# Performance work log

Measured on AMD Instinct MI355X. Metric: run time of the kernel, lower is better.

The kernel has to match this reference:

```python
import jax, jax.numpy as jnp
import numpy as np

NBITS = 4
QMAX = 2 ** (NBITS - 1) - 1   # 7
QMIN = -(2 ** (NBITS - 1))    # -8


def quantize_weight(W):
    # Brevitas-style symmetric per-tensor int4 weight quantization with STE.
    scale = jnp.max(jnp.abs(W)) / QMAX
    q = jnp.clip(jnp.round(W / scale), QMIN, QMAX) * scale
    # straight-through estimator (no-op for fwd-only, kept for parity)
    return W + jax.lax.stop_gradient(q - W)


def setup_inputs() -> dict:
    key = jax.random.key(0)
    k1, k2, k3 = jax.random.split(key, 3)
    x = jax.random.normal(k1, (8192, 4, 16, 16, 16), dtype=jnp.float32)
    W = jax.random.normal(k2, (4, 2048), dtype=jnp.float32) * 0.02
    b = jax.random.normal(k3, (4,), dtype=jnp.float32) * 0.01
    return {"x": x, "W": W, "b": b}


def reference(x, W, b):
    B, C, D, H, Wd = x.shape
    # MaxPool3d(kernel=2, stride=2): reshape-and-reduce (dims are divisible by 2)
    pooled = x.reshape(B, C, D // 2, 2, H // 2, 2, Wd // 2, 2).max(axis=(3, 5, 7))
    flat = pooled.reshape(B, -1)                      # [B, 2048]
    Wq = quantize_weight(W)                           # int4-dequantized weight
    logits = jnp.einsum("bf,of->bo", flat, Wq) + b    # [B, 4]
    return jax.nn.softmax(logits, axis=1)
```

## Files before the change

kernel.cpp:

```cpp
#include <hip/hip_runtime.h>
#include <math.h>

__global__ __launch_bounds__(1024) void quant_w_kernel(
        const float* __restrict__ W, float* __restrict__ wqt ) {
    __shared__ float smax[16];
    __shared__ float sscale;
    const int t = threadIdx.x;
    const float4 v0 = ((const float4*)W)[t];
    const float4 v1 = ((const float4*)W)[t + 1024];

    float m = fmaxf(
        fmaxf(fmaxf(fabsf(v0.x), fabsf(v0.y)), fmaxf(fabsf(v0.z), fabsf(v0.w))),
        fmaxf(fmaxf(fabsf(v1.x), fabsf(v1.y)), fmaxf(fabsf(v1.z), fabsf(v1.w))));
    #pragma unroll
    for (int off = 32; off; off >>= 1) m = fmaxf(m, __shfl_xor(m, off));
    if ((t & 63) == 0) smax[t >> 6] = m;
    __syncthreads();
    if (t == 0) {
        float M = smax[0];
        #pragma unroll
        for (int i = 1; i < 16; ++i) M = fmaxf(M, smax[i]);
        sscale = M / 7.0f;
    }
    __syncthreads();
    const float scale = sscale;

#define QSTORE(val, idx)                                              \
    {                                                                 \
        const int i_ = (idx);                                         \
        const int o_ = i_ >> 11;             \
        const int f_ = i_ & 2047;                        \
        float q_ = rintf((val) / scale);    \
        q_ = fminf(fmaxf(q_, -8.0f), 7.0f);                           \
        wqt[f_ * 4 + o_] = q_ * scale;                                \
    }
    const int i0 = t << 2;
    QSTORE(v0.x, i0 + 0); QSTORE(v0.y, i0 + 1);
    QSTORE(v0.z, i0 + 2); QSTORE(v0.w, i0 + 3);
    QSTORE(v1.x, i0 + 4096); QSTORE(v1.y, i0 + 4097);
    QSTORE(v1.z, i0 + 4098); QSTORE(v1.w, i0 + 4099);
#undef QSTORE
}

__global__ __launch_bounds__(256) void fused_pool_linear_softmax(
        const float* __restrict__ x,
        const float* __restrict__ wqt,
        const float* __restrict__ bias,
        float* __restrict__ out) {
    const int t  = threadIdx.x;
    const int wv = t >> 6;
    const int l  = t & 63;
    const int b  = (blockIdx.x << 2) + wv;

    const float* __restrict__ p = x + (size_t)b * 16384 + (l << 2);
    const int hodd = (l >> 2) & 1;
    const int f0   = hodd * 64 + (l >> 3) * 8 + ((l & 3) << 1);
    const float* __restrict__ wp = wqt + f0 * 4;

    float4 acc = make_float4(0.f, 0.f, 0.f, 0.f);

    #pragma unroll 4
    for (int it = 0; it < 16; ++it) {
        const float4 v0 = *(const float4*)(p);
        const float4 v1 = *(const float4*)(p + 256);
        const float4 v2 = *(const float4*)(p + 512);
        const float4 v3 = *(const float4*)(p + 768);
        p += 1024;

        const float aA = fmaxf(fmaxf(v0.x, v0.y), fmaxf(v1.x, v1.y));
        const float bA = fmaxf(fmaxf(v0.z, v0.w), fmaxf(v1.z, v1.w));
        const float aB = fmaxf(fmaxf(v2.x, v2.y), fmaxf(v3.x, v3.y));
        const float bB = fmaxf(fmaxf(v2.z, v2.w), fmaxf(v3.z, v3.w));

        const float saA = __shfl_xor(aA, 4);
        const float sbA = __shfl_xor(bA, 4);
        const float saB = __shfl_xor(aB, 4);
        const float sbB = __shfl_xor(bB, 4);

        const float p0 = hodd ? fmaxf(aB, saB) : fmaxf(aA, saA);
        const float p1 = hodd ? fmaxf(bB, sbB) : fmaxf(bA, sbA);

        const float4 w0 = *(const float4*)(wp);
        const float4 w1 = *(const float4*)(wp + 4);
        wp += 512;

        acc.x = fmaf(p0, w0.x, fmaf(p1, w1.x, acc.x));
        acc.y = fmaf(p0, w0.y, fmaf(p1, w1.y, acc.y));
        acc.z = fmaf(p0, w0.z, fmaf(p1, w1.z, acc.z));
        acc.w = fmaf(p0, w0.w, fmaf(p1, w1.w, acc.w));
    }

    #pragma unroll
    for (int off = 32; off; off >>= 1) {
        acc.x += __shfl_xor(acc.x, off);
        acc.y += __shfl_xor(acc.y, off);
        acc.z += __shfl_xor(acc.z, off);
        acc.w += __shfl_xor(acc.w, off);
    }

    if (l == 0) {
        const float4 bi = *(const float4*)bias;
        const float l0 = acc.x + bi.x, l1 = acc.y + bi.y,
                    l2 = acc.z + bi.z, l3 = acc.w + bi.w;
        const float m  = fmaxf(fmaxf(l0, l1), fmaxf(l2, l3));
        const float e0 = expf(l0 - m), e1 = expf(l1 - m),
                    e2 = expf(l2 - m), e3 = expf(l3 - m);
        const float inv = 1.0f / (e0 + e1 + e2 + e3);
        *(float4*)(out + (size_t)b * 4) =
            make_float4(e0 * inv, e1 * inv, e2 * inv, e3 * inv);
    }
}

extern "C" void kernel_launch(void* const* d_in, const int* in_sizes, int n_in,
                              void* d_out, int out_size, void* d_ws, size_t ws_size,
                              hipStream_t stream) {
    const float* x    = (const float*)d_in[0];
    const float* W    = (const float*)d_in[1];
    const float* bias = (const float*)d_in[2];
    float* out = (float*)d_out;
    float* wqt = (float*)d_ws;

    quant_w_kernel<<<1, 1024, 0, stream>>>(W, wqt);
    fused_pool_linear_softmax<<<2048, 256, 0, stream>>>(x, wqt, bias, out);
}
```

Before: 682.6 us.

## Fuse weight quantization into main kernel with per-block LDS weight copy

```diff
diff --git a/kernel.cpp b/kernel.cpp
--- a/kernel.cpp
+++ b/kernel.cpp
@@ -1,61 +1,57 @@
 #include <hip/hip_runtime.h>
 #include <math.h>
 
-__global__ __launch_bounds__(1024) void quant_w_kernel(
-        const float* __restrict__ W, float* __restrict__ wqt ) {
-    __shared__ float smax[16];
-    __shared__ float sscale;
+__global__ __launch_bounds__(512) void fused_all(
+        const float* __restrict__ x,
+        const float* __restrict__ W,
+        const float* __restrict__ bias,
+        float* __restrict__ out) {
+    __shared__ float wlds[2048 * 4];
+    __shared__ float smax[8];
+
     const int t = threadIdx.x;
-    const float4 v0 = ((const float4*)W)[t];
-    const float4 v1 = ((const float4*)W)[t + 1024];
+    const int l = t & 63;
 
-    float m = fmaxf(
-        fmaxf(fmaxf(fabsf(v0.x), fabsf(v0.y)), fmaxf(fabsf(v0.z), fabsf(v0.w))),
-        fmaxf(fmaxf(fabsf(v1.x), fabsf(v1.y)), fmaxf(fabsf(v1.z), fabsf(v1.w))));
+    float4 wv[4];
+    float m = 0.0f;
+    #pragma unroll
+    for (int i = 0; i < 4; ++i) {
+        wv[i] = ((const float4*)W)[t + 512 * i];
+        m = fmaxf(m, fmaxf(fmaxf(fabsf(wv[i].x), fabsf(wv[i].y)),
+                           fmaxf(fabsf(wv[i].z), fabsf(wv[i].w))));
+    }
     #pragma unroll
     for (int off = 32; off; off >>= 1) m = fmaxf(m, __shfl_xor(m, off));
-    if ((t & 63) == 0) smax[t >> 6] = m;
+    if (l == 0) smax[t >> 6] = m;
     __syncthreads();
-    if (t == 0) {
-        float M = smax[0];
-        #pragma unroll
-        for (int i = 1; i < 16; ++i) M = fmaxf(M, smax[i]);
-        sscale = M / 7.0f;
-    }
-    __syncthreads();
-    const float scale = sscale;
+    float M = smax[0];
+    #pragma unroll
+    for (int i = 1; i < 8; ++i) M = fmaxf(M, smax[i]);
+    const float scale = M / 7.0f;
 
-#define QSTORE(val, idx)                                              \
+#define QSTORE(val, gidx)                                             \
     {                                                                 \
-        const int i_ = (idx);                                         \
-        const int o_ = i_ >> 11;             \
-        const int f_ = i_ & 2047;                        \
+        const int g_ = (gidx);                                        \
         float q_ = rintf((val) / scale);    \
         q_ = fminf(fmaxf(q_, -8.0f), 7.0f);                           \
-        wqt[f_ * 4 + o_] = q_ * scale;                                \
+        wlds[(g_ & 2047) * 4 + (g_ >> 11)] = q_ * scale;              \
     }
-    const int i0 = t << 2;
-    QSTORE(v0.x, i0 + 0); QSTORE(v0.y, i0 + 1);
-    QSTORE(v0.z, i0 + 2); QSTORE(v0.w, i0 + 3);
-    QSTORE(v1.x, i0 + 4096); QSTORE(v1.y, i0 + 4097);
-    QSTORE(v1.z, i0 + 4098); QSTORE(v1.w, i0 + 4099);
+    #pragma unroll
+    for (int i = 0; i < 4; ++i) {
+        const int g0 = (t + 512 * i) << 2;
+        QSTORE(wv[i].x, g0 + 0); QSTORE(wv[i].y, g0 + 1);
+        QSTORE(wv[i].z, g0 + 2); QSTORE(wv[i].w, g0 + 3);
+    }
 #undef QSTORE
-}
+    __syncthreads();
 
-__global__ __launch_bounds__(256) void fused_pool_linear_softmax(
-        const float* __restrict__ x,
-        const float* __restrict__ wqt,
-        const float* __restrict__ bias,
-        float* __restrict__ out) {
-    const int t  = threadIdx.x;
-    const int wv = t >> 6;
-    const int l  = t & 63;
-    const int b  = (blockIdx.x << 2) + wv;
+    const int wv_id = t >> 6;
+    const int b     = (blockIdx.x << 3) + wv_id;
 
     const float* __restrict__ p = x + (size_t)b * 16384 + (l << 2);
     const int hodd = (l >> 2) & 1;
     const int f0   = hodd * 64 + (l >> 3) * 8 + ((l & 3) << 1);
-    const float* __restrict__ wp = wqt + f0 * 4;
+    const float* wl = wlds + f0 * 4;
 
     float4 acc = make_float4(0.f, 0.f, 0.f, 0.f);
 
@@ -80,9 +76,9 @@
         const float p0 = hodd ? fmaxf(aB, saB) : fmaxf(aA, saA);
         const float p1 = hodd ? fmaxf(bB, sbB) : fmaxf(bA, sbA);
 
-        const float4 w0 = *(const float4*)(wp);
-        const float4 w1 = *(const float4*)(wp + 4);
-        wp += 512;
+        const float4 w0 = *(const float4*)(wl);
+        const float4 w1 = *(const float4*)(wl + 4);
+        wl += 512;
 
         acc.x = fmaf(p0, w0.x, fmaf(p1, w1.x, acc.x));
         acc.y = fmaf(p0, w0.y, fmaf(p1, w1.y, acc.y));
@@ -102,9 +98,9 @@
         const float4 bi = *(const float4*)bias;
         const float l0 = acc.x + bi.x, l1 = acc.y + bi.y,
                     l2 = acc.z + bi.z, l3 = acc.w + bi.w;
-        const float m  = fmaxf(fmaxf(l0, l1), fmaxf(l2, l3));
-        const float e0 = expf(l0 - m), e1 = expf(l1 - m),
-                    e2 = expf(l2 - m), e3 = expf(l3 - m);
+        const float mm = fmaxf(fmaxf(l0, l1), fmaxf(l2, l3));
+        const float e0 = expf(l0 - mm), e1 = expf(l1 - mm),
+                    e2 = expf(l2 - mm), e3 = expf(l3 - mm);
         const float inv = 1.0f / (e0 + e1 + e2 + e3);
         *(float4*)(out + (size_t)b * 4) =
             make_float4(e0 * inv, e1 * inv, e2 * inv, e3 * inv);
@@ -118,8 +114,7 @@
     const float* W    = (const float*)d_in[1];
     const float* bias = (const float*)d_in[2];
     float* out = (float*)d_out;
-    float* wqt = (float*)d_ws;
+    (void)d_ws; (void)ws_size;
 
-    quant_w_kernel<<<1, 1024, 0, stream>>>(W, wqt);
-    fused_pool_linear_softmax<<<2048, 256, 0, stream>>>(x, wqt, bias, out);
+    fused_all<<<1024, 512, 0, stream>>>(x, W, bias, out);
 }
```

New measurement: 690.2 us. No clear change (+1.1%).
